# Performance work log

Hardware: AMD Instinct MI355X
Metric: run time of the kernel (lower is better)

The kernel has to match this reference:

```python
import jax, jax.numpy as jnp
import numpy as np

PH, PW = 7, 7  # pooled_height, pooled_width
B, H, W, C, R = 4, 64, 64, 256, 128


def setup_inputs() -> dict:
    key = jax.random.key(0)
    k1, k2, k3 = jax.random.split(key, 3)
    feature_map = jax.random.normal(k1, (B, H, W, C), dtype=jnp.float32)
    # ROIs: (y_min, x_min, y_max, x_max) relative coords; sized so every
    # region has >= PH rows / PW cols (avoids empty-bin -inf edge case).
    start = jax.random.uniform(k2, (B, R, 2), minval=0.0, maxval=0.4)
    extent = jax.random.uniform(k3, (B, R, 2), minval=0.3, maxval=0.55)
    rois = jnp.concatenate([start, start + extent], axis=-1).astype(jnp.float32)
    return {"feature_map": feature_map, "rois": rois}


def _pool_image(fm, rois_img):
    # fm: (H, W, C); rois_img: (R, 4)
    h, w, _ = fm.shape
    # tf.cast(float->int32) truncates; coords are non-negative so == floor
    h0 = jnp.floor(h * rois_img[:, 0]).astype(jnp.int32)
    w0 = jnp.floor(w * rois_img[:, 1]).astype(jnp.int32)
    h1 = jnp.floor(h * rois_img[:, 2]).astype(jnp.int32)
    w1 = jnp.floor(w * rois_img[:, 3]).astype(jnp.int32)
    rh, rw = h1 - h0, w1 - w0
    hstep = jnp.maximum(rh // PH, 1)  # guard: assumes region >= pooled grid
    wstep = jnp.maximum(rw // PW, 1)

    # Map each absolute row/col to its pooled bin (or PH/PW = "outside").
    rel_h = jnp.arange(h)[None, :] - h0[:, None]            # (R, H)
    bin_h = jnp.clip(rel_h // hstep[:, None], 0, PH - 1)     # last bin extends to region end
    row_id = jnp.where((rel_h >= 0) & (rel_h < rh[:, None]), bin_h, PH)
    rel_w = jnp.arange(w)[None, :] - w0[:, None]            # (R, W)
    bin_w = jnp.clip(rel_w // wstep[:, None], 0, PW - 1)
    col_id = jnp.where((rel_w >= 0) & (rel_w < rw[:, None]), bin_w, PW)

    # Stage 1: segment-max over rows -> (R, PH, W, C)
    seg_rows = jax.vmap(
        lambda ids: jax.ops.segment_max(fm, ids, num_segments=PH + 1)
    )(row_id)[:, :PH]

    # Stage 2: segment-max over cols -> (R, PH, PW, C)
    def col_pool(t, ids):  # t: (PH, W, C)
        tt = jnp.swapaxes(t, 0, 1)  # (W, PH, C)
        s = jax.ops.segment_max(tt, ids, num_segments=PW + 1)[:PW]
        return jnp.swapaxes(s, 0, 1)  # (PH, PW, C)

    return jax.vmap(col_pool)(seg_rows, col_id)


def reference(feature_map, rois):
    # (B, R, PH, PW, C)
    return jax.vmap(_pool_image)(feature_map, rois)
```

## Files before the change

kernel.cpp:

```cpp
#include <hip/hip_runtime.h>
#include <math.h>

#define PH 7
#define PW 7
#define BB 4
#define HH 64
#define WW 64
#define CC 256
#define RR 128
#define CH4 (CC / 4)
#define BINS_PER_IMG (RR * PH * PW)
#define NBINS (BB * BINS_PER_IMG)
#define NBLK (NBINS / 4)
#define BLK_PER_IMG (NBLK / 8)

typedef float f4 __attribute__((ext_vector_type(4)));

__device__ __forceinline__ f4 max4(f4 a, f4 b) {
    f4 r;
    r.x = fmaxf(a.x, b.x); r.y = fmaxf(a.y, b.y);
    r.z = fmaxf(a.z, b.z); r.w = fmaxf(a.w, b.w);
    return r;
}

__global__ __launch_bounds__(256) void ROIPoolingLayer_62079457296467_kernel(
    const float* __restrict__ fm, const float* __restrict__ rois,
    float* __restrict__ out)
{
    const int wave = threadIdx.x >> 6;
    const int lane = threadIdx.x & 63;

    const int bid   = blockIdx.x;
    const int xcd   = bid & 7;
    const int slot  = bid >> 3;
    const int b     = xcd >> 1;
    const int blkin = (xcd & 1) * BLK_PER_IMG + slot;
    const int local = blkin * 4 + wave;
    const int r     = local / (PH * PW);
    const int bin   = local - r * (PH * PW);
    const int ph    = bin / PW;
    const int pw    = bin - ph * PW;
    const int br    = b * RR + r;

    const f4 roi = ((const f4*)rois)[br];
    const int h0 = (int)floorf((float)HH * roi.x);
    const int w0 = (int)floorf((float)WW * roi.y);
    const int h1 = (int)floorf((float)HH * roi.z);
    const int w1 = (int)floorf((float)WW * roi.w);
    const int rh = h1 - h0;
    const int rw = w1 - w0;
    const int hstep = max(rh / PH, 1);
    const int wstep = max(rw / PW, 1);

    int hs = h0 + ph * hstep;
    int he = (ph == PH - 1) ? (h0 + rh) : (hs + hstep);
    he = min(he, h0 + rh);  he = min(he, HH);
    int ws = w0 + pw * wstep;
    int we = (pw == PW - 1) ? (w0 + rw) : (ws + wstep);
    we = min(we, w0 + rw);  we = min(we, WW);

    const int hbin = he - hs;
    const int wbin = we - ws;
    const int npix = hbin * wbin;

    const f4* __restrict__ fmb =
        (const f4*)fm + ((size_t)b * HH + hs) * (WW * CH4) + (size_t)ws * CH4 + lane;

    f4 acc = (f4){-INFINITY, -INFINITY, -INFINITY, -INFINITY};

    if (npix > 0) {
        const unsigned m = (65536u + (unsigned)wbin - 1) / (unsigned)wbin;
        for (int p = 0; p < npix; p += 8) {
            f4 v[8];
#pragma unroll
            for (int k = 0; k < 8; ++k) {
                const int pk = min(p + k, npix - 1);
                const int q  = (int)(((unsigned)pk * m) >> 16);
                const int w  = pk - q * wbin;
                v[k] = fmb[((size_t)q * WW + w) * CH4];
            }
#pragma unroll
            for (int k = 0; k < 8; ++k)
                acc = max4(acc, v[k]);
        }
    }

    const size_t gbin = (size_t)b * BINS_PER_IMG + local;
    __builtin_nontemporal_store(acc, (f4*)out + gbin * CH4 + lane);
}

extern "C" void kernel_launch(void* const* d_in, const int* in_sizes, int n_in,
                              void* d_out, int out_size, void* d_ws, size_t ws_size,
                              hipStream_t stream) {
    const float* fm   = (const float*)d_in[0];
    const float* rois = (const float*)d_in[1];
    float* out        = (float*)d_out;
    ROIPoolingLayer_62079457296467_kernel<<<NBLK, 256, 0, stream>>>(fm, rois, out);
}
```

Baseline: 89.37 us.

## Precompute 2x2 max-pooled pyramid and pool ROI bins from it plus edges

Adds a pre-pass kernel that builds a 2x2 max-reduced copy of the feature map in workspace. Each ROI bin then reads its 2x2-aligned interior from that copy and only the odd border rows and columns from the full-resolution map, cutting the number of loads per bin roughly fourfold for large bins. It also makes offsets wave-uniform via readfirstlane and uses a tree-shaped max reduction. The cost is an extra kernel launch plus a full read of the feature map and a write of the pyramid. It keeps a direct-path fallback for when the workspace is too small.

```diff
diff --git a/kernel.cpp b/kernel.cpp
--- a/kernel.cpp
+++ b/kernel.cpp
@@ -13,6 +13,9 @@
 #define NBINS (BB * BINS_PER_IMG)
 #define NBLK (NBINS / 4)
 #define BLK_PER_IMG (NBLK / 8)
+#define P2H 32
+#define P2W 32
+#define P2_BYTES ((size_t)BB * P2H * P2W * CC * 4)
 
 typedef float f4 __attribute__((ext_vector_type(4)));
 
@@ -22,35 +25,49 @@
     r.z = fmaxf(a.z, b.z); r.w = fmaxf(a.w, b.w);
     return r;
 }
+__device__ __forceinline__ int rfl(int x) { return __builtin_amdgcn_readfirstlane(x); }
+
+__global__ __launch_bounds__(256) void build_p2_kernel(
+    const float* __restrict__ fm, float* __restrict__ p2)
+{
+    const int lane = threadIdx.x & 63;
+    const int wave = rfl((int)threadIdx.x >> 6);
+    const int bid  = blockIdx.x;
+    const int xcd  = bid & 7;
+    const int b    = xcd >> 1;
+    const int idx  = (xcd & 1) * 128 + (bid >> 3);
+    const int local = idx * 4 + wave;
+    const int h2 = local >> 5, w2 = local & 31;
+
+    const f4* src = (const f4*)fm + (((size_t)b * HH + 2 * h2) * WW + 2 * w2) * CH4 + lane;
+    f4 v0 = src[0], v1 = src[CH4], v2 = src[WW * CH4], v3 = src[WW * CH4 + CH4];
+    ((f4*)p2)[((size_t)b * (P2H * P2W) + local) * CH4 + lane] = max4(max4(v0, v1), max4(v2, v3));
+}
 
 __global__ __launch_bounds__(256) void ROIPoolingLayer_62079457296467_kernel(
     const float* __restrict__ fm, const float* __restrict__ rois,
-    float* __restrict__ out)
+    const float* __restrict__ p2, float* __restrict__ out)
 {
-    const int wave = threadIdx.x >> 6;
     const int lane = threadIdx.x & 63;
+    const int wave = rfl((int)threadIdx.x >> 6);
 
     const int bid   = blockIdx.x;
     const int xcd   = bid & 7;
-    const int slot  = bid >> 3;
     const int b     = xcd >> 1;
-    const int blkin = (xcd & 1) * BLK_PER_IMG + slot;
+    const int blkin = (xcd & 1) * BLK_PER_IMG + (bid >> 3);
     const int local = blkin * 4 + wave;
     const int r     = local / (PH * PW);
     const int bin   = local - r * (PH * PW);
     const int ph    = bin / PW;
     const int pw    = bin - ph * PW;
-    const int br    = b * RR + r;
-
-    const f4 roi = ((const f4*)rois)[br];
-    const int h0 = (int)floorf((float)HH * roi.x);
-    const int w0 = (int)floorf((float)WW * roi.y);
-    const int h1 = (int)floorf((float)HH * roi.z);
-    const int w1 = (int)floorf((float)WW * roi.w);
-    const int rh = h1 - h0;
-    const int rw = w1 - w0;
-    const int hstep = max(rh / PH, 1);
-    const int wstep = max(rw / PW, 1);
+
+    const f4 roi = ((const f4*)rois)[b * RR + r];
+    const int h0 = rfl((int)floorf((float)HH * roi.x));
+    const int w0 = rfl((int)floorf((float)WW * roi.y));
+    const int h1 = rfl((int)floorf((float)HH * roi.z));
+    const int w1 = rfl((int)floorf((float)WW * roi.w));
+    const int rh = h1 - h0, rw = w1 - w0;
+    const int hstep = max(rh / PH, 1), wstep = max(rw / PW, 1);
 
     int hs = h0 + ph * hstep;
     int he = (ph == PH - 1) ? (h0 + rh) : (hs + hstep);
@@ -59,15 +76,121 @@
     int we = (pw == PW - 1) ? (w0 + rw) : (ws + wstep);
     we = min(we, w0 + rw);  we = min(we, WW);
 
-    const int hbin = he - hs;
-    const int wbin = we - ws;
-    const int npix = hbin * wbin;
-
-    const f4* __restrict__ fmb =
-        (const f4*)fm + ((size_t)b * HH + hs) * (WW * CH4) + (size_t)ws * CH4 + lane;
-
+    const f4* fmb = (const f4*)fm + (size_t)b * (HH * WW) * CH4 + lane;
+    const f4* p2b = (const f4*)p2 + (size_t)b * (P2H * P2W) * CH4 + lane;
     f4 acc = (f4){-INFINITY, -INFINITY, -INFINITY, -INFINITY};
 
+    if (he > hs && we > ws) {
+        const int wbin = we - ws;
+        const int h2s = (hs + 1) >> 1, h2e = he >> 1;
+        const int w2s = (ws + 1) >> 1, w2e = we >> 1;
+        const int n2h = max(h2e - h2s, 0), n2w = max(w2e - w2s, 0);
+        const int il0 = 2 * h2s, il1 = max(2 * h2e, il0);
+        const int jl0 = 2 * w2s, jl1 = max(2 * w2e, jl0);
+
+        const int nint = n2h * n2w;
+        if (nint > 0) {
+            const unsigned m = (65536u + (unsigned)n2w - 1) / (unsigned)n2w;
+            for (int p = 0; p < nint; p += 8) {
+                f4 v[8];
+#pragma unroll
+                for (int k = 0; k < 8; ++k) {
+                    const int pk = min(p + k, nint - 1);
+                    const int q  = (int)(((unsigned)pk * m) >> 16);
+                    const int c  = pk - q * n2w;
+                    const int off = rfl((h2s + q) * P2W + (w2s + c));
+                    v[k] = p2b[(size_t)off * CH4];
+                }
+#pragma unroll
+                for (int k = 0; k < 4; ++k) v[k] = max4(v[k], v[k + 4]);
+                acc = max4(acc, max4(max4(v[0], v[1]), max4(v[2], v[3])));
+            }
+        }
+
+        const int t1 = min(il0, he);
+        const int b0 = max(il1, hs);
+        const int nt = max(t1 - hs, 0), nb = max(he - b0, 0);
+        const int nrow = nt + nb;
+        const int rowA = nt ? hs : b0, rowB = b0;
+        const int nhe = nrow * wbin;
+        if (nhe > 0) {
+            const unsigned m = (65536u + (unsigned)wbin - 1) / (unsigned)wbin;
+            for (int p = 0; p < nhe; p += 8) {
+                f4 v[8];
+#pragma unroll
+                for (int k = 0; k < 8; ++k) {
+                    const int pk = min(p + k, nhe - 1);
+                    const int q  = (int)(((unsigned)pk * m) >> 16);
+                    const int rr2 = q ? rowB : rowA;
+                    const int c  = ws + (pk - q * wbin);
+                    const int off = rfl(rr2 * WW + c);
+                    v[k] = fmb[(size_t)off * CH4];
+                }
+#pragma unroll
+                for (int k = 0; k < 4; ++k) v[k] = max4(v[k], v[k + 4]);
+                acc = max4(acc, max4(max4(v[0], v[1]), max4(v[2], v[3])));
+            }
+        }
+
+        const int ilen = il1 - il0;
+        const int nl = max(min(jl0, we) - ws, 0);
+        const int nr = max(we - max(jl1, ws), 0);
+        const int ncols = nl + nr;
+        const int colA = nl ? ws : (we - 1), colB = we - 1;
+        const int nve = ilen * ncols;
+        if (nve > 0) {
+            for (int p = 0; p < nve; p += 8) {
+                f4 v[8];
+#pragma unroll
+                for (int k = 0; k < 8; ++k) {
+                    const int pk = min(p + k, nve - 1);
+                    const int hh = il0 + ((ncols == 2) ? (pk >> 1) : pk);
+                    const int c  = (ncols == 2 && (pk & 1)) ? colB : colA;
+                    const int off = rfl(hh * WW + c);
+                    v[k] = fmb[(size_t)off * CH4];
+                }
+#pragma unroll
+                for (int k = 0; k < 4; ++k) v[k] = max4(v[k], v[k + 4]);
+                acc = max4(acc, max4(max4(v[0], v[1]), max4(v[2], v[3])));
+            }
+        }
+    }
+
+    const size_t gbin = (size_t)b * BINS_PER_IMG + local;
+    __builtin_nontemporal_store(acc, (f4*)out + gbin * CH4 + lane);
+}
+
+__global__ __launch_bounds__(256) void roi_direct_kernel(
+    const float* __restrict__ fm, const float* __restrict__ rois,
+    float* __restrict__ out)
+{
+    const int lane = threadIdx.x & 63;
+    const int wave = rfl((int)threadIdx.x >> 6);
+    const int bid   = blockIdx.x;
+    const int xcd   = bid & 7;
+    const int b     = xcd >> 1;
+    const int blkin = (xcd & 1) * BLK_PER_IMG + (bid >> 3);
+    const int local = blkin * 4 + wave;
+    const int r     = local / (PH * PW);
+    const int bin   = local - r * (PH * PW);
+    const int ph    = bin / PW;
+    const int pw    = bin - ph * PW;
+    const f4 roi = ((const f4*)rois)[b * RR + r];
+    const int h0 = rfl((int)floorf((float)HH * roi.x));
+    const int w0 = rfl((int)floorf((float)WW * roi.y));
+    const int h1 = rfl((int)floorf((float)HH * roi.z));
+    const int w1 = rfl((int)floorf((float)WW * roi.w));
+    const int rh = h1 - h0, rw = w1 - w0;
+    const int hstep = max(rh / PH, 1), wstep = max(rw / PW, 1);
+    int hs = h0 + ph * hstep;
+    int he = (ph == PH - 1) ? (h0 + rh) : (hs + hstep);
+    he = min(he, h0 + rh);  he = min(he, HH);
+    int ws = w0 + pw * wstep;
+    int we = (pw == PW - 1) ? (w0 + rw) : (ws + wstep);
+    we = min(we, w0 + rw);  we = min(we, WW);
+    const int wbin = we - ws, npix = (he - hs) * wbin;
+    const f4* fmb = (const f4*)fm + (((size_t)b * HH + hs) * WW + ws) * CH4 + lane;
+    f4 acc = (f4){-INFINITY, -INFINITY, -INFINITY, -INFINITY};
     if (npix > 0) {
         const unsigned m = (65536u + (unsigned)wbin - 1) / (unsigned)wbin;
         for (int p = 0; p < npix; p += 8) {
@@ -76,15 +199,14 @@
             for (int k = 0; k < 8; ++k) {
                 const int pk = min(p + k, npix - 1);
                 const int q  = (int)(((unsigned)pk * m) >> 16);
-                const int w  = pk - q * wbin;
-                v[k] = fmb[((size_t)q * WW + w) * CH4];
-            }
-#pragma unroll
-            for (int k = 0; k < 8; ++k)
-                acc = max4(acc, v[k]);
+                const int off = rfl(q * WW + (pk - q * wbin));
+                v[k] = fmb[(size_t)off * CH4];
+            }
+#pragma unroll
+            for (int k = 0; k < 4; ++k) v[k] = max4(v[k], v[k + 4]);
+            acc = max4(acc, max4(max4(v[0], v[1]), max4(v[2], v[3])));
         }
     }
-
     const size_t gbin = (size_t)b * BINS_PER_IMG + local;
     __builtin_nontemporal_store(acc, (f4*)out + gbin * CH4 + lane);
 }
@@ -95,5 +217,11 @@
     const float* fm   = (const float*)d_in[0];
     const float* rois = (const float*)d_in[1];
     float* out        = (float*)d_out;
-    ROIPoolingLayer_62079457296467_kernel<<<NBLK, 256, 0, stream>>>(fm, rois, out);
-}
+    if (ws_size >= P2_BYTES) {
+        float* p2 = (float*)d_ws;
+        build_p2_kernel<<<1024, 256, 0, stream>>>(fm, p2);
+        ROIPoolingLayer_62079457296467_kernel<<<NBLK, 256, 0, stream>>>(fm, rois, p2, out);
+    } else {
+        roi_direct_kernel<<<NBLK, 256, 0, stream>>>(fm, rois, out);
+    }
+}
```

Result: slower. 97.03 us (+8.6%).
